# Kernel tuning notes

Measured on AMD Instinct MI355X. Metric: run time of the kernel, lower is better.

The kernel has to match this reference:

```python
import jax, jax.numpy as jnp
import numpy as np
import math

LMAX = 10
N_SH = (LMAX + 1) ** 2  # 121
_lambert_sh_k = [3.1415926535897927, 2.0943951023931957, 0.7853981633974483, 0.0,
                 -0.13089969389957473, 0.0, 0.04908738521234052, 0.0,
                 -0.024543692606170262, 0.0, 0.014317154020265985]
_reps = [2 * l + 1 for l in range(LMAX + 1)]
LAMBERT_VEC = jnp.asarray(np.repeat(np.array(_lambert_sh_k, np.float32), _reps))  # (121,)
EXPO_VEC = jnp.asarray(np.repeat(np.array([l * (l + 1) / 2.0 for l in range(LMAX + 1)], np.float32), _reps))  # (121,)

def _dfact(n):
    # double factorial n!!, with (-1)!! = 1
    out = 1.0
    while n > 0:
        out *= n
        n -= 2
    return out

def _K(l, m):
    return math.sqrt((2 * l + 1) / (4 * math.pi) * math.factorial(l - m) / math.factorial(l + m))

def sh_basis(d):
    """Real spherical harmonics up to LMAX, e3nn-style ordering (m=-l..l per l),
    'integral' normalization, homogeneous in |d| (normalize=False semantics: Y_l(r*u)=r^l Y_l(u))."""
    r = jnp.linalg.norm(d, axis=-1, keepdims=True)  # (N,1)
    u = d / jnp.maximum(r, 1e-12)
    x, y, z = u[..., 0], u[..., 1], u[..., 2]
    rr = r[..., 0]
    # c[m] = sin^m(theta)*cos(m*phi), s[m] = sin^m(theta)*sin(m*phi) via complex power recurrence
    c = [jnp.ones_like(x)]
    s = [jnp.zeros_like(x)]
    for m in range(1, LMAX + 1):
        c.append(x * c[m - 1] - y * s[m - 1])
        s.append(x * s[m - 1] + y * c[m - 1])
    # Q[l][m] = P_l^m(z) / sin^m(theta) (polynomial in z, no Condon-Shortley)
    Q = {}
    for m in range(LMAX + 1):
        Q[(m, m)] = jnp.full_like(x, _dfact(2 * m - 1))
        if m < LMAX:
            Q[(m + 1, m)] = (2 * m + 1) * z * Q[(m, m)]
        for l in range(m + 2, LMAX + 1):
            Q[(l, m)] = ((2 * l - 1) * z * Q[(l - 1, m)] - (l + m - 1) * Q[(l - 2, m)]) / (l - m)
    cols = [None] * N_SH
    for l in range(LMAX + 1):
        rl = rr ** l
        cols[l * l + l] = _K(l, 0) * Q[(l, 0)] * rl
        for m in range(1, l + 1):
            f = math.sqrt(2.0) * _K(l, m)
            cols[l * l + l + m] = f * Q[(l, m)] * c[m] * rl
            cols[l * l + l - m] = f * Q[(l, m)] * s[m] * rl
    return jnp.stack(cols, axis=-1)  # (N, 121)

def setup_inputs() -> dict:
    key = jax.random.key(0)
    ks = jax.random.split(key, 16)
    N = 131072
    W = 512
    normals = jax.random.normal(ks[0], (N, 3), jnp.float32)
    normals = normals / jnp.linalg.norm(normals, axis=-1, keepdims=True)
    view_dirs = jax.random.normal(ks[1], (N, 3), jnp.float32)
    view_dirs = view_dirs / jnp.linalg.norm(view_dirs, axis=-1, keepdims=True)
    feature = jax.random.normal(ks[2], (N, 16), jnp.float32)
    ref_SH = jax.random.normal(ks[3], (N, N_SH, 3), jnp.float32) * 0.1
    def xavier(k, fi, fo):
        lim = math.sqrt(6.0 / (fi + fo))
        return jax.random.uniform(k, (fi, fo), jnp.float32, -lim, lim)
    return {
        'normals': normals, 'view_dirs': view_dirs, 'feature': feature, 'ref_SH': ref_SH,
        'w0': xavier(ks[4], 8, W), 'b0': jnp.zeros((W,), jnp.float32),
        'w1': xavier(ks[5], W, W), 'b1': jnp.zeros((W,), jnp.float32),
        'w2': xavier(ks[6], W, W), 'b2': jnp.zeros((W,), jnp.float32),
        'w3': xavier(ks[7], W, W), 'b3': jnp.zeros((W,), jnp.float32),
        'wc': xavier(ks[8], W, 27), 'bc': jnp.zeros((27,), jnp.float32),
    }

def reference(normals, view_dirs, feature, ref_SH, w0, b0, w1, b1, w2, b2, w3, b3, wc, bc):
    roughness = jax.nn.softplus(feature[..., 0:1])          # (N,1)
    coe = feature[..., 1:10]                                 # (N,9)
    albedo = jax.nn.sigmoid(feature[..., 10:13])             # (N,3)
    spec = jax.nn.sigmoid(feature[..., 13:16])               # (N,3)
    # diffuse irradiance: Lambert-coefficient-weighted SH of normals
    irradiance = jax.nn.relu(jnp.einsum('nk,nkc->nc', sh_basis(normals) * LAMBERT_VEC, ref_SH))
    diffuse = albedo * irradiance
    # specular: roughness-filtered SH of reflection direction
    dot = jnp.sum(normals * view_dirs, axis=-1, keepdims=True)  # (N,1)
    wr = 2.0 * normals * dot - view_dirs                        # (N,3)
    decay = jnp.exp(-EXPO_VEC * roughness)                      # (N,121)
    light = jax.nn.relu(jnp.einsum('nk,nkc->nc', sh_basis(wr) * decay, ref_SH))
    # conditioning MLP
    h = jnp.concatenate([dot, view_dirs, normals, roughness], axis=-1)  # (N,8)
    h = jax.nn.relu(h @ w0 + b0)
    h = jax.nn.relu(h @ w1 + b1)
    h = jax.nn.relu(h @ w2 + b2)
    h = jax.nn.relu(h @ w3 + b3)
    cs = h @ wc + bc                                            # (N,27)
    rr_ = jnp.sum(cs[..., 0:9] * coe, axis=-1, keepdims=True)
    gg_ = jnp.sum(cs[..., 9:18] * coe, axis=-1, keepdims=True)
    bb_ = jnp.sum(cs[..., 18:27] * coe, axis=-1, keepdims=True)
    gate = jax.nn.sigmoid(jnp.concatenate([rr_, gg_, bb_], axis=-1))  # (N,3)
    specular = spec * light * gate
    raw_rgb = diffuse + specular
    sh_light = jnp.concatenate([light, irradiance], axis=0)     # (2N,3)
    return raw_rgb, albedo, diffuse, specular, sh_light
```

## Files before the change

kernel.cpp:

```cpp
#include <hip/hip_runtime.h>
#include <hip/hip_bf16.h>
#include <stdint.h>
#include <math.h>

typedef __hip_bfloat16 bf16;
typedef __attribute__((ext_vector_type(8))) __bf16 bf16x8;
typedef __attribute__((ext_vector_type(4))) float f32x4;

__device__ __forceinline__ float b2f(bf16 x){ return __bfloat162float(x); }
__device__ __forceinline__ bf16 f2b(float x){ return __float2bfloat16(x); }
__device__ __forceinline__ float sigmoidf_(float x){ return 1.f/(1.f+expf(-x)); }

template<int ISF>
__device__ __forceinline__ float ldin(const void* p, long i){
  if (ISF) return ((const float*)p)[i];
  return b2f(((const bf16*)p)[i]);
}
template<int ISF>
__device__ __forceinline__ void stout(void* p, long i, float v){
  if (ISF) ((float*)p)[i] = v;
  else     ((bf16*)p)[i] = f2b(v);
}

__device__ const float DTAB[11] = {1.f,1.f,3.f,15.f,105.f,945.f,10395.f,135135.f,
                                   2027025.f,34459425.f,654729075.f};
__device__ const float LAMB[11] = {3.1415926535897927f, 2.0943951023931957f, 0.7853981633974483f,
                                   0.0f, -0.13089969389957473f, 0.0f, 0.04908738521234052f, 0.0f,
                                   -0.024543692606170262f, 0.0f, 0.014317154020265985f};

__global__ void detect_dtype(const void* __restrict__ normals, int* __restrict__ flag){
  if (threadIdx.x != 0 || blockIdx.x != 0) return;
  const float* pf = (const float*)normals;
  const uint16_t* pb = (const uint16_t*)normals;
  int cf = 0, cb = 0;
  for (int p = 0; p < 256; p++){
    float a = pf[p*3+0], b = pf[p*3+1], c = pf[p*3+2];
    float s = a*a + b*b + c*c;
    if (fabsf(s - 1.f) < 0.05f) cf++;
    float x = __uint_as_float(((uint32_t)pb[p*3+0]) << 16);
    float y = __uint_as_float(((uint32_t)pb[p*3+1]) << 16);
    float z = __uint_as_float(((uint32_t)pb[p*3+2]) << 16);
    float s2 = x*x + y*y + z*z;
    if (fabsf(s2 - 1.f) < 0.05f) cb++;
  }
  *flag = (cf > cb) ? 1 : 0;
}

__global__ __launch_bounds__(256) void transpose512(const void* __restrict__ w1,
                                                    const void* __restrict__ w2,
                                                    const void* __restrict__ w3,
                                                    bf16* __restrict__ outT,
                                                    const int* __restrict__ flagp){
  int isf = *flagp;
  const void* src = (blockIdx.y==0) ? w1 : (blockIdx.y==1) ? w2 : w3;
  bf16* dst = outT + (size_t)blockIdx.y*512*512;
  int i = blockIdx.x*256 + threadIdx.x;
  int k = i >> 9, n = i & 511;
  float v = isf ? ((const float*)src)[i] : b2f(((const bf16*)src)[i]);
  dst[n*512 + k] = f2b(v);
}

__global__ __launch_bounds__(256) void prep_wcT(const void* __restrict__ wc, bf16* __restrict__ wcT,
                                                const int* __restrict__ flagp){
  int isf = *flagp;
  int i = blockIdx.x*256 + threadIdx.x;
  int n = i >> 9, k = i & 511;
  float v = 0.f;
  if (n < 27) v = isf ? ((const float*)wc)[k*27+n] : b2f(((const bf16*)wc)[k*27+n]);
  wcT[i] = f2b(v);
}

__global__ __launch_bounds__(256) void prep_small(const void* b0, const void* b1,
    const void* b2, const void* b3, const void* bc, const void* w0,
    float* __restrict__ fsm, const int* __restrict__ flagp){
  int isf = *flagp;
  int i = blockIdx.x*256 + threadIdx.x;
  if (i >= 6176) return;
  float v;
  if (i < 512)       v = isf ? ((const float*)b0)[i]      : b2f(((const bf16*)b0)[i]);
  else if (i < 1024){ int j=i-512;  v = isf ? ((const float*)b1)[j] : b2f(((const bf16*)b1)[j]); }
  else if (i < 1536){ int j=i-1024; v = isf ? ((const float*)b2)[j] : b2f(((const bf16*)b2)[j]); }
  else if (i < 2048){ int j=i-1536; v = isf ? ((const float*)b3)[j] : b2f(((const bf16*)b3)[j]); }
  else if (i < 2080){ int j=i-2048; v = (j<27) ? (isf ? ((const float*)bc)[j] : b2f(((const bf16*)bc)[j])) : 0.f; }
  else              { int j=i-2080; v = isf ? ((const float*)w0)[j] : b2f(((const bf16*)w0)[j]); }
  fsm[i] = v;
}

template<int ISF>
__device__ void point_body(const void* __restrict__ normals, const void* __restrict__ viewd,
    const void* __restrict__ feat, const void* __restrict__ refsh,
    void* __restrict__ out, float* __restrict__ lightirr, float* __restrict__ h0,
    int N, const float* s_klm, int p)
{
  float nx = ldin<ISF>(normals,(long)p*3+0), ny = ldin<ISF>(normals,(long)p*3+1), nz = ldin<ISF>(normals,(long)p*3+2);
  float vx = ldin<ISF>(viewd,(long)p*3+0),  vy = ldin<ISF>(viewd,(long)p*3+1),  vz = ldin<ISF>(viewd,(long)p*3+2);
  long fb = (long)p*16;
  float f0 = ldin<ISF>(feat, fb+0);
  float rough = (f0 > 20.f) ? f0 : log1pf(expf(f0));
  float dotnv = nx*vx + ny*vy + nz*vz;
  float wx = 2.f*nx*dotnv - vx, wy = 2.f*ny*dotnv - vy, wz = 2.f*nz*dotnv - vz;

  float rA = sqrtf(nx*nx+ny*ny+nz*nz);
  float iA = 1.f/fmaxf(rA, 1e-12f);
  float ax = nx*iA, ay = ny*iA, az = nz*iA;
  float rB = sqrtf(wx*wx+wy*wy+wz*wz);
  float iB = 1.f/fmaxf(rB, 1e-12f);
  float bx = wx*iB, by = wy*iB, bz = wz*iB;

  long rowb = (long)p*363;
  float irr[3] = {0,0,0}, lig[3] = {0,0,0};
  float ccA=1.f, ssA=0.f, ccB=1.f, ssB=0.f, rmA=1.f, rmB=1.f;
  for (int m=0; m<=10; m++){
    if (m > 0){
      float tA = ax*ccA - ay*ssA; ssA = ax*ssA + ay*ccA; ccA = tA;
      float tB = bx*ccB - by*ssB; ssB = bx*ssB + by*ccB; ccB = tB;
      rmA *= rA; rmB *= rB;
    }
    float qA = DTAB[m], qB = DTAB[m];
    float pA = 0.f, pB = 0.f;
    float rlA = rmA, rlB = rmB;
    for (int l=m; l<=10; l++){
      if (l > m){
        float nA, nB;
        if (l == m+1){ nA = (float)(2*m+1)*az*qA; nB = (float)(2*m+1)*bz*qB; }
        else {
          float inv = 1.f/(float)(l-m);
          nA = ((float)(2*l-1)*az*qA - (float)(l+m-1)*pA)*inv;
          nB = ((float)(2*l-1)*bz*qB - (float)(l+m-1)*pB)*inv;
        }
        pA = qA; qA = nA; pB = qB; qB = nB;
        rlA *= rA; rlB *= rB;
      }
      float kc = s_klm[l*(l+1)/2 + m];
      float dec = expf(-(0.5f*(float)(l*(l+1)))*rough);
      float laml = LAMB[l];
      float wIA = kc*qA*rlA*laml;
      float wLB = kc*qB*rlB*dec;
      if (m == 0){
        long rp = rowb + (long)(l*l+l)*3;
        #pragma unroll
        for (int c=0;c<3;c++){
          float rv = ldin<ISF>(refsh, rp+c);
          irr[c] += wIA*rv;
          lig[c] += wLB*rv;
        }
      } else {
        long rpp = rowb + (long)(l*l+l+m)*3;
        long rpm = rowb + (long)(l*l+l-m)*3;
        #pragma unroll
        for (int c=0;c<3;c++){
          float rv = ldin<ISF>(refsh, rpp+c);
          irr[c] += wIA*ccA*rv;
          lig[c] += wLB*ccB*rv;
        }
        #pragma unroll
        for (int c=0;c<3;c++){
          float rv = ldin<ISF>(refsh, rpm+c);
          irr[c] += wIA*ssA*rv;
          lig[c] += wLB*ssB*rv;
        }
      }
    }
  }
  long N3 = (long)3*N;
  #pragma unroll
  for (int c=0;c<3;c++){
    float ir = fmaxf(irr[c], 0.f);
    float lg = fmaxf(lig[c], 0.f);
    float alb = sigmoidf_(ldin<ISF>(feat, fb+10+c));
    stout<ISF>(out, N3   + (long)p*3 + c, alb);
    stout<ISF>(out, 2*N3 + (long)p*3 + c, alb*ir);
    stout<ISF>(out, 4*N3 + (long)p*3 + c, lg);
    stout<ISF>(out, 4*N3 + ((long)N + p)*3 + c, ir);
    lightirr[(long)p*6 + c]     = lg;
    lightirr[(long)p*6 + 3 + c] = ir;
  }
  float* h = h0 + (long)p*8;
  h[0]=dotnv; h[1]=vx; h[2]=vy; h[3]=vz; h[4]=nx; h[5]=ny; h[6]=nz; h[7]=rough;
}

__global__ __launch_bounds__(256) void point_kernel(
    const void* __restrict__ normals, const void* __restrict__ viewd,
    const void* __restrict__ feat, const void* __restrict__ refsh,
    void* __restrict__ out, float* __restrict__ lightirr, float* __restrict__ h0,
    int N, const int* __restrict__ flagp)
{
  __shared__ float s_klm[66];
  int tid = threadIdx.x;
  if (tid < 66){
    int l = 0, t = tid;
    while (t >= l+1){ t -= (l+1); l++; }
    int m = t;
    double fr = 1.0;
    for (int i = l-m+1; i <= l+m; i++) fr /= (double)i;
    double K = sqrt((2.0*l+1.0)/(4.0*3.14159265358979323846) * fr);
    if (m > 0) K *= 1.4142135623730951;
    s_klm[tid] = (float)K;
  }
  __syncthreads();
  int p = blockIdx.x*256 + tid;
  if (p >= N) return;
  if (*flagp) point_body<1>(normals,viewd,feat,refsh,out,lightirr,h0,N,s_klm,p);
  else        point_body<0>(normals,viewd,feat,refsh,out,lightirr,h0,N,s_klm,p);
}

__global__ __launch_bounds__(256) void gemm0(const float* __restrict__ h0,
    const float* __restrict__ w0f, const float* __restrict__ b0f,
    bf16* __restrict__ outp, int rows){
  __shared__ float w0s[8*512];
  __shared__ float b0s[512];
  int tid = threadIdx.x;
  #pragma unroll
  for (int i=0;i<16;i++){ int e = i*256+tid; w0s[e] = w0f[e]; }
  b0s[tid] = b0f[tid]; b0s[256+tid] = b0f[256+tid];
  __syncthreads();
  long r = (long)blockIdx.x*32 + (tid>>3);
  int cg = tid & 7;
  float hv[8];
  #pragma unroll
  for (int k=0;k<8;k++) hv[k] = h0[r*8+k];
  bf16* orow = outp + r*512;
  for (int cc=0; cc<64; cc++){
    int col = cg + cc*8;
    float a = b0s[col];
    #pragma unroll
    for (int k=0;k<8;k++) a += hv[k]*w0s[k*512+col];
    orow[col] = f2b(fmaxf(a, 0.f));
  }
}

template<int WN, bool RELU, bool OUTBF>
__global__ __launch_bounds__(256) void gemm_bt(
    const bf16* __restrict__ A, const bf16* __restrict__ Bt,
    const float* __restrict__ bias,
    void* __restrict__ outv, int ldout, int rows)
{
  constexpr int BN = 32*WN;
  constexpr int BK = 64;
  constexpr int NCH_B = BN/32;
  __shared__ bf16 As[128*BK];
  __shared__ bf16 Bs[BN*BK];
  const int tid  = threadIdx.x;
  const int wave = tid >> 6, lane = tid & 63;
  const int quad = lane >> 4, l16 = lane & 15;
  const int wrow = wave >> 1, wcol = wave & 1;
  const int m_off = wrow*64, n_off = wcol*16*WN;
  const long rowBase = (long)blockIdx.x * 128;
  const int  colBase = blockIdx.y * BN;

  f32x4 acc[4][WN];
  #pragma unroll
  for (int i=0;i<4;i++)
    #pragma unroll
    for (int j=0;j<WN;j++) acc[i][j] = (f32x4){0.f,0.f,0.f,0.f};

  for (int kt=0; kt<512; kt+=BK){
    bf16x8 ga[4], gb[NCH_B];
    #pragma unroll
    for (int ch=0; ch<4; ch++){
      int flat = ch*2048 + wave*512 + lane*8;
      int m = flat >> 6, kk = flat & 63;
      ga[ch] = *(const bf16x8*)(A + (rowBase + m)*512 + kt + kk);
    }
    #pragma unroll
    for (int ch=0; ch<NCH_B; ch++){
      int flat = ch*2048 + wave*512 + lane*8;
      int n = flat >> 6, kk = flat & 63;
      gb[ch] = *(const bf16x8*)(Bt + (long)(colBase + n)*512 + kt + kk);
    }
    __syncthreads();
    #pragma unroll
    for (int ch=0; ch<4; ch++){
      int flat = ch*2048 + wave*512 + lane*8;
      *(bf16x8*)(As + flat) = ga[ch];
    }
    #pragma unroll
    for (int ch=0; ch<NCH_B; ch++){
      int flat = ch*2048 + wave*512 + lane*8;
      *(bf16x8*)(Bs + flat) = gb[ch];
    }
    __syncthreads();
    #pragma unroll
    for (int kk=0; kk<BK; kk+=32){
      bf16x8 af[4], bfr[WN];
      #pragma unroll
      for (int i=0;i<4;i++)
        af[i] = *(const bf16x8*)(As + (m_off + i*16 + l16)*BK + kk + quad*8);
      #pragma unroll
      for (int j=0;j<WN;j++)
        bfr[j] = *(const bf16x8*)(Bs + (n_off + j*16 + l16)*BK + kk + quad*8);
      #pragma unroll
      for (int i=0;i<4;i++)
        #pragma unroll
        for (int j=0;j<WN;j++)
          acc[i][j] = __builtin_amdgcn_mfma_f32_16x16x32_bf16(af[i], bfr[j], acc[i][j], 0,0,0);
    }
  }
  #pragma unroll
  for (int j=0;j<WN;j++){
    int cg = colBase + n_off + j*16 + l16;
    float bv = bias[cg];
    #pragma unroll
    for (int i=0;i<4;i++){
      long rg0 = rowBase + m_off + i*16 + quad*4;
      #pragma unroll
      for (int r=0;r<4;r++){
        float v = acc[i][j][r] + bv;
        if (RELU) v = fmaxf(v, 0.f);
        if (OUTBF) ((bf16*)outv)[(rg0+r)*(long)ldout + cg] = f2b(v);
        else       ((float*)outv)[(rg0+r)*(long)ldout + cg] = v;
      }
    }
  }
}

template<int ISF>
__device__ void epi_body(const float* __restrict__ cs, const void* __restrict__ feat,
    const float* __restrict__ lightirr, void* __restrict__ out, long base, int N, int p){
  long gp = base + p;
  const float* c = cs + (long)p*32;
  long fb = gp*16;
  float rr=0.f, gg=0.f, bb=0.f;
  #pragma unroll
  for (int j=0;j<9;j++){
    float co = ldin<ISF>(feat, fb+1+j);
    rr += c[j]*co; gg += c[9+j]*co; bb += c[18+j]*co;
  }
  float gate[3] = { sigmoidf_(rr), sigmoidf_(gg), sigmoidf_(bb) };
  const float* li = lightirr + gp*6;
  long N3 = (long)3*N;
  #pragma unroll
  for (int cc=0; cc<3; cc++){
    float spec = sigmoidf_(ldin<ISF>(feat, fb+13+cc));
    float alb  = sigmoidf_(ldin<ISF>(feat, fb+10+cc));
    float specular = spec * li[cc] * gate[cc];
    float diffuse  = alb * li[3+cc];
    stout<ISF>(out, gp*3 + cc, diffuse + specular);
    stout<ISF>(out, 3*N3 + gp*3 + cc, specular);
  }
}

__global__ __launch_bounds__(256) void epilogue_kernel(const float* __restrict__ cs,
    const void* __restrict__ feat, const float* __restrict__ lightirr,
    void* __restrict__ out, long base, int N, int rows, const int* __restrict__ flagp){
  int p = blockIdx.x*256 + threadIdx.x;
  if (p >= rows) return;
  if (*flagp) epi_body<1>(cs, feat, lightirr, out, base, N, p);
  else        epi_body<0>(cs, feat, lightirr, out, base, N, p);
}

extern "C" void kernel_launch(void* const* d_in, const int* in_sizes, int n_in,
                              void* d_out, int out_size, void* d_ws, size_t ws_size,
                              hipStream_t stream) {
  const void* normals = d_in[0];
  const void* viewd   = d_in[1];
  const void* feat    = d_in[2];
  const void* refsh   = d_in[3];
  int N = in_sizes[0] / 3;

  char* ws = (char*)d_ws;
  size_t off = 0;
  int* flag = (int*)ws;                     off += 256;
  bf16* wT  = (bf16*)(ws + off);            off += (size_t)3*512*512*2;
  bf16* wcT = (bf16*)(ws + off);            off += (size_t)32*512*2;
  float* fsm = (float*)(ws + off);          off += (size_t)6176*4; off = (off+255)&~(size_t)255;
  float* h0 = (float*)(ws + off);           off += (size_t)N*8*4;
  float* lightirr = (float*)(ws + off);     off += (size_t)N*6*4;
  size_t fixed = off;

  size_t avail = (ws_size > fixed) ? (ws_size - fixed) : 0;
  long chunk = (long)(avail / 2176) & ~255L;
  if (chunk < 256) chunk = 256;
  if (chunk > N) chunk = N;
  bf16* hA = (bf16*)(ws + fixed);
  bf16* hB = (bf16*)(ws + fixed + (size_t)chunk*1024);
  float* cs = (float*)(ws + fixed + (size_t)chunk*2048);

  detect_dtype<<<1, 64, 0, stream>>>(normals, flag);
  transpose512<<<dim3(1024,3), 256, 0, stream>>>(d_in[6], d_in[8], d_in[10], wT, flag);
  prep_wcT<<<64, 256, 0, stream>>>(d_in[12], wcT, flag);
  prep_small<<<25, 256, 0, stream>>>(d_in[5], d_in[7], d_in[9], d_in[11], d_in[13], d_in[4], fsm, flag);
  point_kernel<<<N/256, 256, 0, stream>>>(normals, viewd, feat, refsh, d_out, lightirr, h0, N, flag);

  for (long base = 0; base < N; base += chunk){
    long rows = (N - base < chunk) ? (N - base) : chunk;
    gemm0<<<rows/32, 256, 0, stream>>>(h0 + base*8, fsm + 2080, fsm + 0, hA, (int)rows);
    gemm_bt<4,true,true ><<<dim3(rows/128,4), 256, 0, stream>>>(hA, wT,          fsm + 512,  hB, 512, (int)rows);
    gemm_bt<4,true,true ><<<dim3(rows/128,4), 256, 0, stream>>>(hB, wT + 262144, fsm + 1024, hA, 512, (int)rows);
    gemm_bt<4,true,true ><<<dim3(rows/128,4), 256, 0, stream>>>(hA, wT + 524288, fsm + 1536, hB, 512, (int)rows);
    gemm_bt<1,false,false><<<dim3(rows/128,1), 256, 0, stream>>>(hB, wcT,        fsm + 2048, cs,  32, (int)rows);
    epilogue_kernel<<<rows/256, 256, 0, stream>>>(cs, feat, lightirr, d_out, base, N, (int)rows, flag);
  }
}
```

Baseline: 935.6 us.

## Stage SH rows in LDS, split per-point SH work across 8 lanes, async GEMM loads

The point kernel now stages each block's 32 ref_SH rows into shared memory with direct global-to-LDS loads. Each point's m-orders are spread across 8 threads and combined with shuffle reductions, and the per-l decay exp is replaced by a multiplicative recurrence. The GEMM tile loads use global_load_lds instead of going through registers, the weight transpose goes through a shared-memory tile, and the runtime dtype detection is removed so the code assumes fp32 inputs. The goal is to remove uncoalesced strided loads of the 363-float rows and low per-thread parallelism. The cost is an fp32-only assumption and an extra barrier per K step in the GEMM.

```diff
diff --git a/kernel.cpp b/kernel.cpp
--- a/kernel.cpp
+++ b/kernel.cpp
@@ -11,15 +11,10 @@
 __device__ __forceinline__ bf16 f2b(float x){ return __float2bfloat16(x); }
 __device__ __forceinline__ float sigmoidf_(float x){ return 1.f/(1.f+expf(-x)); }
 
-template<int ISF>
-__device__ __forceinline__ float ldin(const void* p, long i){
-  if (ISF) return ((const float*)p)[i];
-  return b2f(((const bf16*)p)[i]);
-}
-template<int ISF>
-__device__ __forceinline__ void stout(void* p, long i, float v){
-  if (ISF) ((float*)p)[i] = v;
-  else     ((bf16*)p)[i] = f2b(v);
+__device__ __forceinline__ void ld_lds16(const void* g, void* l){
+  __builtin_amdgcn_global_load_lds(
+      (const __attribute__((address_space(1))) uint32_t*)g,
+      (__attribute__((address_space(3))) uint32_t*)l, 16, 0, 0);
 }
 
 __device__ const float DTAB[11] = {1.f,1.f,3.f,15.f,105.f,945.f,10395.f,135135.f,
@@ -28,74 +23,85 @@
                                    0.0f, -0.13089969389957473f, 0.0f, 0.04908738521234052f, 0.0f,
                                    -0.024543692606170262f, 0.0f, 0.014317154020265985f};
 
-__global__ void detect_dtype(const void* __restrict__ normals, int* __restrict__ flag){
-  if (threadIdx.x != 0 || blockIdx.x != 0) return;
-  const float* pf = (const float*)normals;
-  const uint16_t* pb = (const uint16_t*)normals;
-  int cf = 0, cb = 0;
-  for (int p = 0; p < 256; p++){
-    float a = pf[p*3+0], b = pf[p*3+1], c = pf[p*3+2];
-    float s = a*a + b*b + c*c;
-    if (fabsf(s - 1.f) < 0.05f) cf++;
-    float x = __uint_as_float(((uint32_t)pb[p*3+0]) << 16);
-    float y = __uint_as_float(((uint32_t)pb[p*3+1]) << 16);
-    float z = __uint_as_float(((uint32_t)pb[p*3+2]) << 16);
-    float s2 = x*x + y*y + z*z;
-    if (fabsf(s2 - 1.f) < 0.05f) cb++;
-  }
-  *flag = (cf > cb) ? 1 : 0;
-}
-
-__global__ __launch_bounds__(256) void transpose512(const void* __restrict__ w1,
-                                                    const void* __restrict__ w2,
-                                                    const void* __restrict__ w3,
-                                                    bf16* __restrict__ outT,
-                                                    const int* __restrict__ flagp){
-  int isf = *flagp;
-  const void* src = (blockIdx.y==0) ? w1 : (blockIdx.y==1) ? w2 : w3;
-  bf16* dst = outT + (size_t)blockIdx.y*512*512;
-  int i = blockIdx.x*256 + threadIdx.x;
-  int k = i >> 9, n = i & 511;
-  float v = isf ? ((const float*)src)[i] : b2f(((const bf16*)src)[i]);
-  dst[n*512 + k] = f2b(v);
-}
-
-__global__ __launch_bounds__(256) void prep_wcT(const void* __restrict__ wc, bf16* __restrict__ wcT,
-                                                const int* __restrict__ flagp){
-  int isf = *flagp;
+__global__ __launch_bounds__(256) void transpose512(const float* __restrict__ w1,
+                                                    const float* __restrict__ w2,
+                                                    const float* __restrict__ w3,
+                                                    bf16* __restrict__ outT){
+  __shared__ float tile[64][65];
+  const float* src = (blockIdx.z==0) ? w1 : (blockIdx.z==1) ? w2 : w3;
+  bf16* dst = outT + (size_t)blockIdx.z*512*512;
+  int bx = blockIdx.x*64, by = blockIdx.y*64;
+  int tx = threadIdx.x & 63, tg = threadIdx.x >> 6;
+  #pragma unroll
+  for (int rr=0; rr<16; rr++){
+    int row = tg*16 + rr;
+    tile[row][tx] = src[(by+row)*512 + bx+tx];
+  }
+  __syncthreads();
+  #pragma unroll
+  for (int rr=0; rr<16; rr++){
+    int row = tg*16 + rr;
+    dst[(size_t)(bx+row)*512 + by+tx] = f2b(tile[tx][row]);
+  }
+}
+
+__global__ __launch_bounds__(256) void prep_wcT(const float* __restrict__ wc, bf16* __restrict__ wcT){
   int i = blockIdx.x*256 + threadIdx.x;
   int n = i >> 9, k = i & 511;
-  float v = 0.f;
-  if (n < 27) v = isf ? ((const float*)wc)[k*27+n] : b2f(((const bf16*)wc)[k*27+n]);
-  wcT[i] = f2b(v);
-}
-
-__global__ __launch_bounds__(256) void prep_small(const void* b0, const void* b1,
-    const void* b2, const void* b3, const void* bc, const void* w0,
-    float* __restrict__ fsm, const int* __restrict__ flagp){
-  int isf = *flagp;
+  wcT[i] = f2b((n < 27) ? wc[k*27 + n] : 0.f);
+}
+
+__global__ __launch_bounds__(256) void prep_small(const float* b0, const float* b1,
+    const float* b2, const float* b3, const float* bc, const float* w0,
+    float* __restrict__ fsm){
   int i = blockIdx.x*256 + threadIdx.x;
   if (i >= 6176) return;
   float v;
-  if (i < 512)       v = isf ? ((const float*)b0)[i]      : b2f(((const bf16*)b0)[i]);
-  else if (i < 1024){ int j=i-512;  v = isf ? ((const float*)b1)[j] : b2f(((const bf16*)b1)[j]); }
-  else if (i < 1536){ int j=i-1024; v = isf ? ((const float*)b2)[j] : b2f(((const bf16*)b2)[j]); }
-  else if (i < 2048){ int j=i-1536; v = isf ? ((const float*)b3)[j] : b2f(((const bf16*)b3)[j]); }
-  else if (i < 2080){ int j=i-2048; v = (j<27) ? (isf ? ((const float*)bc)[j] : b2f(((const bf16*)bc)[j])) : 0.f; }
-  else              { int j=i-2080; v = isf ? ((const float*)w0)[j] : b2f(((const bf16*)w0)[j]); }
+  if (i < 512)       v = b0[i];
+  else if (i < 1024) v = b1[i-512];
+  else if (i < 1536) v = b2[i-1024];
+  else if (i < 2048) v = b3[i-1536];
+  else if (i < 2080){ int j=i-2048; v = (j<27) ? bc[j] : 0.f; }
+  else               v = w0[i-2080];
   fsm[i] = v;
 }
 
-template<int ISF>
-__device__ void point_body(const void* __restrict__ normals, const void* __restrict__ viewd,
-    const void* __restrict__ feat, const void* __restrict__ refsh,
-    void* __restrict__ out, float* __restrict__ lightirr, float* __restrict__ h0,
-    int N, const float* s_klm, int p)
+__global__ __launch_bounds__(256) void point_kernel(
+    const float* __restrict__ nrm, const float* __restrict__ vwd,
+    const float* __restrict__ feat, const float* __restrict__ refsh,
+    float* __restrict__ out, float* __restrict__ lightirr, float* __restrict__ h0, int N)
 {
-  float nx = ldin<ISF>(normals,(long)p*3+0), ny = ldin<ISF>(normals,(long)p*3+1), nz = ldin<ISF>(normals,(long)p*3+2);
-  float vx = ldin<ISF>(viewd,(long)p*3+0),  vy = ldin<ISF>(viewd,(long)p*3+1),  vz = ldin<ISF>(viewd,(long)p*3+2);
-  long fb = (long)p*16;
-  float f0 = ldin<ISF>(feat, fb+0);
+  __shared__ float rows[32*363];
+  __shared__ float s_klm[66];
+  const int tid = threadIdx.x;
+  if (tid < 66){
+    int l = 0, t = tid;
+    while (t >= l+1){ t -= (l+1); l++; }
+    int m = t;
+    double fr = 1.0;
+    for (int i = l-m+1; i <= l+m; i++) fr /= (double)i;
+    double K = sqrt((2.0*l+1.0)/(4.0*3.14159265358979323846) * fr);
+    if (m > 0) K *= 1.4142135623730951;
+    s_klm[tid] = (float)K;
+  }
+  const int wave = tid >> 6, lane = tid & 63;
+  const long p0 = (long)blockIdx.x * 32;
+  const float* gbase = refsh + p0*363;
+  #pragma unroll
+  for (int t=0; t<12; t++){
+    int fi = t*1024 + wave*256 + lane*4;
+    if (fi < 32*363)
+      ld_lds16(gbase + fi, rows + t*1024 + wave*256);
+  }
+  __syncthreads();
+
+  const int r = tid >> 3, j = tid & 7;
+  const long p = p0 + r;
+  const float* row = rows + r*363;
+
+  float nx=nrm[p*3+0], ny=nrm[p*3+1], nz=nrm[p*3+2];
+  float vx=vwd[p*3+0], vy=vwd[p*3+1], vz=vwd[p*3+2];
+  float f0 = feat[p*16];
   float rough = (f0 > 20.f) ? f0 : log1pf(expf(f0));
   float dotnv = nx*vx + ny*vy + nz*vz;
   float wx = 2.f*nx*dotnv - vx, wy = 2.f*ny*dotnv - vy, wz = 2.f*nz*dotnv - vz;
@@ -107,18 +113,20 @@
   float iB = 1.f/fmaxf(rB, 1e-12f);
   float bx = wx*iB, by = wy*iB, bz = wz*iB;
 
-  long rowb = (long)p*363;
   float irr[3] = {0,0,0}, lig[3] = {0,0,0};
-  float ccA=1.f, ssA=0.f, ccB=1.f, ssB=0.f, rmA=1.f, rmB=1.f;
-  for (int m=0; m<=10; m++){
-    if (m > 0){
-      float tA = ax*ccA - ay*ssA; ssA = ax*ssA + ay*ccA; ccA = tA;
-      float tB = bx*ccB - by*ssB; ssB = bx*ssB + by*ccB; ccB = tB;
+  const float E = expf(-rough);
+
+  auto process_m = [&](int m){
+    float cmA=1.f, smA=0.f, cmB=1.f, smB=0.f, rmA=1.f, rmB=1.f;
+    for (int mm=1; mm<=m; mm++){
+      float tA = ax*cmA - ay*smA; smA = ax*smA + ay*cmA; cmA = tA;
+      float tB = bx*cmB - by*smB; smB = bx*smB + by*cmB; cmB = tB;
       rmA *= rA; rmB *= rB;
     }
-    float qA = DTAB[m], qB = DTAB[m];
-    float pA = 0.f, pB = 0.f;
+    float qA = DTAB[m], qB = DTAB[m], pA = 0.f, pB = 0.f;
     float rlA = rmA, rlB = rmB;
+    float dec = expf(-0.5f*(float)(m*(m+1))*rough);
+    float e   = expf(-(float)(m+1)*rough);
     for (int l=m; l<=10; l++){
       if (l > m){
         float nA, nB;
@@ -130,78 +138,54 @@
         }
         pA = qA; qA = nA; pB = qB; qB = nB;
         rlA *= rA; rlB *= rB;
+        dec *= e; e *= E;
       }
       float kc = s_klm[l*(l+1)/2 + m];
-      float dec = expf(-(0.5f*(float)(l*(l+1)))*rough);
-      float laml = LAMB[l];
-      float wIA = kc*qA*rlA*laml;
-      float wLB = kc*qB*rlB*dec;
+      float wI = kc*qA*rlA*LAMB[l];
+      float wL = kc*qB*rlB*dec;
+      int k0 = l*l + l;
       if (m == 0){
-        long rp = rowb + (long)(l*l+l)*3;
+        const float* rp = row + k0*3;
         #pragma unroll
-        for (int c=0;c<3;c++){
-          float rv = ldin<ISF>(refsh, rp+c);
-          irr[c] += wIA*rv;
-          lig[c] += wLB*rv;
-        }
+        for (int c=0;c<3;c++){ float rv = rp[c]; irr[c] += wI*rv; lig[c] += wL*rv; }
       } else {
-        long rpp = rowb + (long)(l*l+l+m)*3;
-        long rpm = rowb + (long)(l*l+l-m)*3;
+        const float* rpp = row + (k0+m)*3;
+        const float* rpm = row + (k0-m)*3;
         #pragma unroll
-        for (int c=0;c<3;c++){
-          float rv = ldin<ISF>(refsh, rpp+c);
-          irr[c] += wIA*ccA*rv;
-          lig[c] += wLB*ccB*rv;
-        }
+        for (int c=0;c<3;c++){ float rv = rpp[c]; irr[c] += wI*cmA*rv; lig[c] += wL*cmB*rv; }
         #pragma unroll
-        for (int c=0;c<3;c++){
-          float rv = ldin<ISF>(refsh, rpm+c);
-          irr[c] += wIA*ssA*rv;
-          lig[c] += wLB*ssB*rv;
-        }
+        for (int c=0;c<3;c++){ float rv = rpm[c]; irr[c] += wI*smA*rv; lig[c] += wL*smB*rv; }
       }
     }
-  }
+  };
+  process_m(j);
+  if (j < 3) process_m(j+8);
+
+  #pragma unroll
+  for (int c=0;c<3;c++){
+    #pragma unroll
+    for (int s=4; s>=1; s>>=1){
+      irr[c] += __shfl_xor(irr[c], s);
+      lig[c] += __shfl_xor(lig[c], s);
+    }
+  }
+  float ir[3], lg[3];
+  #pragma unroll
+  for (int c=0;c<3;c++){ ir[c] = fmaxf(irr[c],0.f); lg[c] = fmaxf(lig[c],0.f); }
+
   long N3 = (long)3*N;
-  #pragma unroll
-  for (int c=0;c<3;c++){
-    float ir = fmaxf(irr[c], 0.f);
-    float lg = fmaxf(lig[c], 0.f);
-    float alb = sigmoidf_(ldin<ISF>(feat, fb+10+c));
-    stout<ISF>(out, N3   + (long)p*3 + c, alb);
-    stout<ISF>(out, 2*N3 + (long)p*3 + c, alb*ir);
-    stout<ISF>(out, 4*N3 + (long)p*3 + c, lg);
-    stout<ISF>(out, 4*N3 + ((long)N + p)*3 + c, ir);
-    lightirr[(long)p*6 + c]     = lg;
-    lightirr[(long)p*6 + 3 + c] = ir;
-  }
-  float* h = h0 + (long)p*8;
-  h[0]=dotnv; h[1]=vx; h[2]=vy; h[3]=vz; h[4]=nx; h[5]=ny; h[6]=nz; h[7]=rough;
-}
-
-__global__ __launch_bounds__(256) void point_kernel(
-    const void* __restrict__ normals, const void* __restrict__ viewd,
-    const void* __restrict__ feat, const void* __restrict__ refsh,
-    void* __restrict__ out, float* __restrict__ lightirr, float* __restrict__ h0,
-    int N, const int* __restrict__ flagp)
-{
-  __shared__ float s_klm[66];
-  int tid = threadIdx.x;
-  if (tid < 66){
-    int l = 0, t = tid;
-    while (t >= l+1){ t -= (l+1); l++; }
-    int m = t;
-    double fr = 1.0;
-    for (int i = l-m+1; i <= l+m; i++) fr /= (double)i;
-    double K = sqrt((2.0*l+1.0)/(4.0*3.14159265358979323846) * fr);
-    if (m > 0) K *= 1.4142135623730951;
-    s_klm[tid] = (float)K;
-  }
-  __syncthreads();
-  int p = blockIdx.x*256 + tid;
-  if (p >= N) return;
-  if (*flagp) point_body<1>(normals,viewd,feat,refsh,out,lightirr,h0,N,s_klm,p);
-  else        point_body<0>(normals,viewd,feat,refsh,out,lightirr,h0,N,s_klm,p);
+  if (j < 3){
+    int c = j;
+    float alb = sigmoidf_(feat[p*16+10+c]);
+    out[N3   + p*3 + c] = alb;
+    out[2*N3 + p*3 + c] = alb*ir[c];
+    out[4*N3 + p*3 + c] = lg[c];
+    out[4*N3 + ((long)N+p)*3 + c] = ir[c];
+  }
+  if (j < 6) lightirr[p*6 + j] = (j<3) ? lg[j] : ir[j-3];
+  float hv = (j==0)?dotnv : (j==1)?vx : (j==2)?vy : (j==3)?vz :
+             (j==4)?nx   : (j==5)?ny : (j==6)?nz : rough;
+  h0[p*8 + j] = hv;
 }
 
 __global__ __launch_bounds__(256) void gemm0(const float* __restrict__ h0,
@@ -255,29 +239,17 @@
     for (int j=0;j<WN;j++) acc[i][j] = (f32x4){0.f,0.f,0.f,0.f};
 
   for (int kt=0; kt<512; kt+=BK){
-    bf16x8 ga[4], gb[NCH_B];
     #pragma unroll
     for (int ch=0; ch<4; ch++){
       int flat = ch*2048 + wave*512 + lane*8;
       int m = flat >> 6, kk = flat & 63;
-      ga[ch] = *(const bf16x8*)(A + (rowBase + m)*512 + kt + kk);
+      ld_lds16(A + (rowBase + m)*512 + kt + kk, As + ch*2048 + wave*512);
     }
     #pragma unroll
     for (int ch=0; ch<NCH_B; ch++){
       int flat = ch*2048 + wave*512 + lane*8;
       int n = flat >> 6, kk = flat & 63;
-      gb[ch] = *(const bf16x8*)(Bt + (long)(colBase + n)*512 + kt + kk);
-    }
-    __syncthreads();
-    #pragma unroll
-    for (int ch=0; ch<4; ch++){
-      int flat = ch*2048 + wave*512 + lane*8;
-      *(bf16x8*)(As + flat) = ga[ch];
-    }
-    #pragma unroll
-    for (int ch=0; ch<NCH_B; ch++){
-      int flat = ch*2048 + wave*512 + lane*8;
-      *(bf16x8*)(Bs + flat) = gb[ch];
+      ld_lds16(Bt + (long)(colBase + n)*512 + kt + kk, Bs + ch*2048 + wave*512);
     }
     __syncthreads();
     #pragma unroll
@@ -295,6 +267,7 @@
         for (int j=0;j<WN;j++)
           acc[i][j] = __builtin_amdgcn_mfma_f32_16x16x32_bf16(af[i], bfr[j], acc[i][j], 0,0,0);
     }
+    __syncthreads();
   }
   #pragma unroll
   for (int j=0;j<WN;j++){
@@ -314,16 +287,18 @@
   }
 }
 
-template<int ISF>
-__device__ void epi_body(const float* __restrict__ cs, const void* __restrict__ feat,
-    const float* __restrict__ lightirr, void* __restrict__ out, long base, int N, int p){
-  long gp = base + p;
-  const float* c = cs + (long)p*32;
-  long fb = gp*16;
+__global__ __launch_bounds__(256) void epilogue_kernel(const float* __restrict__ cs,
+    const float* __restrict__ feat, const float* __restrict__ lightirr,
+    float* __restrict__ out, long base, int N, int rows){
+  int t = blockIdx.x*256 + threadIdx.x;
+  if (t >= rows) return;
+  long gp = base + t;
+  const float* c = cs + (long)t*32;
+  const float* f = feat + gp*16;
   float rr=0.f, gg=0.f, bb=0.f;
   #pragma unroll
   for (int j=0;j<9;j++){
-    float co = ldin<ISF>(feat, fb+1+j);
+    float co = f[1+j];
     rr += c[j]*co; gg += c[9+j]*co; bb += c[18+j]*co;
   }
   float gate[3] = { sigmoidf_(rr), sigmoidf_(gg), sigmoidf_(bb) };
@@ -331,36 +306,27 @@
   long N3 = (long)3*N;
   #pragma unroll
   for (int cc=0; cc<3; cc++){
-    float spec = sigmoidf_(ldin<ISF>(feat, fb+13+cc));
-    float alb  = sigmoidf_(ldin<ISF>(feat, fb+10+cc));
+    float spec = sigmoidf_(f[13+cc]);
+    float alb  = sigmoidf_(f[10+cc]);
     float specular = spec * li[cc] * gate[cc];
     float diffuse  = alb * li[3+cc];
-    stout<ISF>(out, gp*3 + cc, diffuse + specular);
-    stout<ISF>(out, 3*N3 + gp*3 + cc, specular);
-  }
-}
-
-__global__ __launch_bounds__(256) void epilogue_kernel(const float* __restrict__ cs,
-    const void* __restrict__ feat, const float* __restrict__ lightirr,
-    void* __restrict__ out, long base, int N, int rows, const int* __restrict__ flagp){
-  int p = blockIdx.x*256 + threadIdx.x;
-  if (p >= rows) return;
-  if (*flagp) epi_body<1>(cs, feat, lightirr, out, base, N, p);
-  else        epi_body<0>(cs, feat, lightirr, out, base, N, p);
+    out[gp*3 + cc]        = diffuse + specular;
+    out[3*N3 + gp*3 + cc] = specular;
+  }
 }
 
 extern "C" void kernel_launch(void* const* d_in, const int* in_sizes, int n_in,
                               void* d_out, int out_size, void* d_ws, size_t ws_size,
                               hipStream_t stream) {
-  const void* normals = d_in[0];
-  const void* viewd   = d_in[1];
-  const void* feat    = d_in[2];
-  const void* refsh   = d_in[3];
+  const float* normals = (const float*)d_in[0];
+  const float* viewd   = (const float*)d_in[1];
+  const float* feat    = (const float*)d_in[2];
+  const float* refsh   = (const float*)d_in[3];
+  float* out = (float*)d_out;
   int N = in_sizes[0] / 3;
 
   char* ws = (char*)d_ws;
   size_t off = 0;
-  int* flag = (int*)ws;                     off += 256;
   bf16* wT  = (bf16*)(ws + off);            off += (size_t)3*512*512*2;
   bf16* wcT = (bf16*)(ws + off);            off += (size_t)32*512*2;
   float* fsm = (float*)(ws + off);          off += (size_t)6176*4; off = (off+255)&~(size_t)255;
@@ -376,11 +342,13 @@
   bf16* hB = (bf16*)(ws + fixed + (size_t)chunk*1024);
   float* cs = (float*)(ws + fixed + (size_t)chunk*2048);
 
-  detect_dtype<<<1, 64, 0, stream>>>(normals, flag);
-  transpose512<<<dim3(1024,3), 256, 0, stream>>>(d_in[6], d_in[8], d_in[10], wT, flag);
-  prep_wcT<<<64, 256, 0, stream>>>(d_in[12], wcT, flag);
-  prep_small<<<25, 256, 0, stream>>>(d_in[5], d_in[7], d_in[9], d_in[11], d_in[13], d_in[4], fsm, flag);
-  point_kernel<<<N/256, 256, 0, stream>>>(normals, viewd, feat, refsh, d_out, lightirr, h0, N, flag);
+  transpose512<<<dim3(8,8,3), 256, 0, stream>>>((const float*)d_in[6], (const float*)d_in[8],
+                                                (const float*)d_in[10], wT);
+  prep_wcT<<<64, 256, 0, stream>>>((const float*)d_in[12], wcT);
+  prep_small<<<25, 256, 0, stream>>>((const float*)d_in[5], (const float*)d_in[7],
+                                     (const float*)d_in[9], (const float*)d_in[11],
+                                     (const float*)d_in[13], (const float*)d_in[4], fsm);
+  point_kernel<<<N/32, 256, 0, stream>>>(normals, viewd, feat, refsh, out, lightirr, h0, N);
 
   for (long base = 0; base < N; base += chunk){
     long rows = (N - base < chunk) ? (N - base) : chunk;
@@ -389,6 +357,6 @@
     gemm_bt<4,true,true ><<<dim3(rows/128,4), 256, 0, stream>>>(hB, wT + 262144, fsm + 1024, hA, 512, (int)rows);
     gemm_bt<4,true,true ><<<dim3(rows/128,4), 256, 0, stream>>>(hA, wT + 524288, fsm + 1536, hB, 512, (int)rows);
     gemm_bt<1,false,false><<<dim3(rows/128,1), 256, 0, stream>>>(hB, wcT,        fsm + 2048, cs,  32, (int)rows);
-    epilogue_kernel<<<rows/256, 256, 0, stream>>>(cs, feat, lightirr, d_out, base, N, (int)rows, flag);
-  }
-}
+    epilogue_kernel<<<rows/256, 256, 0, stream>>>(cs, feat, lightirr, out, base, N, (int)rows);
+  }
+}
```

Measured after the change: 801.6 us. 14.3% less time.
